# Kernel tuning notes

Hardware: AMD Instinct MI355X
Metric: run time of the kernel (lower is better)

The kernel has to match this reference:

```python
import jax, jax.numpy as jnp
import numpy as np

N = 100000
E = 1600000
IN_C = 128
OUT_C = 64


def setup_inputs() -> dict:
    key = jax.random.key(0)
    ks = jax.random.split(key, 8)
    x = jax.random.normal(ks[0], (N, IN_C), dtype=jnp.float32)
    edge_index = jax.random.randint(ks[1], (2, E), 0, N, dtype=jnp.int64)
    neg_edge_index = jax.random.randint(ks[2], (2, E), 0, N, dtype=jnp.int64)
    # GCNConv params (glorot-ish init)
    W = jax.random.normal(ks[3], (IN_C, OUT_C), dtype=jnp.float32) / np.sqrt(IN_C)
    b = jnp.zeros((OUT_C,), dtype=jnp.float32)
    # classifier Linear(2*out_channels, 2)
    Wc = jax.random.normal(ks[4], (2 * OUT_C, 2), dtype=jnp.float32) / np.sqrt(2 * OUT_C)
    bc = jnp.zeros((2,), dtype=jnp.float32)
    return {"x": x, "edge_index": edge_index, "neg_edge_index": neg_edge_index,
            "W": W, "b": b, "Wc": Wc, "bc": bc}


def gcn_conv(x, edge_index, W, b):
    # Add self-loops, symmetric normalization: D^{-1/2} (A+I) D^{-1/2} X W + b
    loops = jnp.arange(N, dtype=edge_index.dtype)
    src = jnp.concatenate([edge_index[0], loops])  # [E+N]
    dst = jnp.concatenate([edge_index[1], loops])  # [E+N]
    deg = jax.ops.segment_sum(jnp.ones_like(dst, dtype=x.dtype), dst, num_segments=N)
    dinv = jax.lax.rsqrt(jnp.maximum(deg, 1e-12))
    norm = dinv[src] * dinv[dst]                   # [E+N]
    xw = x @ W                                     # [N, OUT_C] transform first (cheaper)
    msg = norm[:, None] * xw[src]                  # gather + scale
    out = jax.ops.segment_sum(msg, dst, num_segments=N)  # scatter-add aggregate
    return out + b


def reference(x, edge_index, neg_edge_index, W, b, Wc, bc):
    h = jax.nn.relu(gcn_conv(x, edge_index, W, b))           # [N, OUT_C]
    total = jnp.concatenate([edge_index, neg_edge_index], axis=1)  # [2, 2E]
    edge_feat = jnp.concatenate([h[total[0]], h[total[1]]], axis=1)  # [2E, 2*OUT_C]
    return edge_feat @ Wc + bc                               # [2E, 2]
```

## Files before the change

### kernel.cpp

```cpp
#include <hip/hip_runtime.h>
#include <stdint.h>

#define N_NODES 100000
#define N_EDGES 1600000
#define IN_C    128
#define OUT_C   64

#define NPB   64
#define NBKT  ((N_NODES + NPB - 1) / NPB)
#define BCAP  1216
#define ACHUNK 8192
#define NABLK ((N_EDGES + ACHUNK - 1) / ACHUNK)

__global__ void zero_kernel(int* __restrict__ cursor) {
    int i = blockIdx.x * blockDim.x + threadIdx.x;
    if (i < NBKT) cursor[i] = 0;
}

__global__ __launch_bounds__(256) void bucketA_kernel(const int* __restrict__ ei,
                                                      int* __restrict__ cursor,
                                                      int* __restrict__ bucket) {
    __shared__ int hist[NBKT];
    __shared__ int base[NBKT];
    __shared__ int hist2[NBKT];
    const int t = threadIdx.x;
    const long long e0 = (long long)blockIdx.x * ACHUNK;
    for (int i = t; i < NBKT; i += 256) { hist[i] = 0; hist2[i] = 0; }
    __syncthreads();
    const int* dsts = ei + N_EDGES;
#pragma unroll
    for (int k = 0; k < ACHUNK / 1024; ++k) {
        long long i4 = e0 / 4 + t + k * 256;
        if (i4 * 4 + 3 < N_EDGES) {
            int4 d = *(const int4*)&dsts[i4 * 4];
            atomicAdd(&hist[d.x >> 6], 1);
            atomicAdd(&hist[d.y >> 6], 1);
            atomicAdd(&hist[d.z >> 6], 1);
            atomicAdd(&hist[d.w >> 6], 1);
        }
    }
    __syncthreads();
    for (int bk = t; bk < NBKT; bk += 256) {
        int c = hist[bk];
        base[bk] = c ? atomicAdd(&cursor[bk], c) : 0;
    }
    __syncthreads();
#pragma unroll
    for (int k = 0; k < ACHUNK / 1024; ++k) {
        long long i4 = e0 / 4 + t + k * 256;
        if (i4 * 4 + 3 < N_EDGES) {
            int4 s4 = *(const int4*)&ei[i4 * 4];
            int4 d4 = *(const int4*)&dsts[i4 * 4];
            int sv[4] = {s4.x, s4.y, s4.z, s4.w};
            int dv[4] = {d4.x, d4.y, d4.z, d4.w};
#pragma unroll
            for (int j = 0; j < 4; ++j) {
                int bk = dv[j] >> 6;
                int pos = base[bk] + atomicAdd(&hist2[bk], 1);
                if (pos < BCAP)
                    bucket[bk * BCAP + pos] = sv[j] * 128 + (dv[j] & (NPB - 1));
            }
        }
    }
}

__global__ __launch_bounds__(256) void bdegcsr_kernel(const int* __restrict__ cursor,
                                                      int* __restrict__ bucket,
                                                      float* __restrict__ dinv,
                                                      int* __restrict__ rowbeg,
                                                      int* __restrict__ rowend) {
    __shared__ int hist[NPB];
    __shared__ int pref[NPB + 1];
    __shared__ int cur[NPB];
    __shared__ int sorted[BCAP];
    const int t = threadIdx.x, b = blockIdx.x;
    if (t < NPB) { hist[t] = 0; cur[t] = 0; }
    __syncthreads();
    int m = cursor[b]; if (m > BCAP) m = BCAP;
    int* bb = bucket + b * BCAP;
    for (int i = t; i < m; i += 256) atomicAdd(&hist[bb[i] & 127], 1);
    __syncthreads();
    if (t == 0) {
        int s = 0;
#pragma unroll
        for (int k = 0; k < NPB; ++k) { pref[k] = s; s += hist[k]; }
        pref[NPB] = s;
    }
    __syncthreads();
    for (int i = t; i < m; i += 256) {
        int e = bb[i];
        int dl = e & 127;
        int pos = pref[dl] + atomicAdd(&cur[dl], 1);
        sorted[pos] = e >> 7;
    }
    __syncthreads();
    for (int i = t; i < m; i += 256) bb[i] = sorted[i];
    if (t < NPB) {
        int n = b * NPB + t;
        if (n < N_NODES) {
            rowbeg[n] = b * BCAP + pref[t];
            rowend[n] = b * BCAP + pref[t + 1];
            dinv[n]   = rsqrtf((float)hist[t] + 1.0f);
        }
    }
}

#define XN  32
#define SXS 132
__global__ __launch_bounds__(256) void xws_kernel(const float* __restrict__ x,
                                                  const float* __restrict__ W,
                                                  const float* __restrict__ dinv,
                                                  float* __restrict__ xws) {
    __shared__ float sW[IN_C * OUT_C];
    __shared__ float sx[XN * SXS];
    const int t = threadIdx.x;
    const int n0 = blockIdx.x * XN;
    const float4* W4 = (const float4*)W;
    float4* sW4 = (float4*)sW;
#pragma unroll
    for (int k = 0; k < 8; ++k) sW4[t + k * 256] = W4[t + k * 256];
#pragma unroll
    for (int k = 0; k < 4; ++k) {
        int idx = (t + k * 256) * 4;
        int r = idx >> 7, kk = idx & 127;
        int n = n0 + r;
        float4 v = (n < N_NODES) ? *(const float4*)&x[(long long)n * IN_C + kk]
                                 : make_float4(0.f, 0.f, 0.f, 0.f);
        *(float4*)&sx[r * SXS + kk] = v;
    }
    __syncthreads();
    const int r  = t >> 4;
    const int cq = (t & 15) << 2;
    float4 a0 = make_float4(0.f,0.f,0.f,0.f), a1 = a0;
#pragma unroll 8
    for (int k = 0; k < IN_C; ++k) {
        float x0 = sx[r * SXS + k];
        float x1 = sx[(r + 16) * SXS + k];
        float4 wv = *(const float4*)&sW[(k << 6) + cq];
        a0.x = fmaf(x0, wv.x, a0.x); a0.y = fmaf(x0, wv.y, a0.y);
        a0.z = fmaf(x0, wv.z, a0.z); a0.w = fmaf(x0, wv.w, a0.w);
        a1.x = fmaf(x1, wv.x, a1.x); a1.y = fmaf(x1, wv.y, a1.y);
        a1.z = fmaf(x1, wv.z, a1.z); a1.w = fmaf(x1, wv.w, a1.w);
    }
    int na = n0 + r, nb = n0 + r + 16;
    if (na < N_NODES) {
        float di = dinv[na];
        a0.x *= di; a0.y *= di; a0.z *= di; a0.w *= di;
        *(float4*)&xws[(long long)na * OUT_C + cq] = a0;
    }
    if (nb < N_NODES) {
        float di = dinv[nb];
        a1.x *= di; a1.y *= di; a1.z *= di; a1.w *= di;
        *(float4*)&xws[(long long)nb * OUT_C + cq] = a1;
    }
}

__global__ __launch_bounds__(256) void aggnode_kernel(
    const int* __restrict__ rowbeg, const int* __restrict__ rowend,
    const int* __restrict__ srcs, const float* __restrict__ dinv,
    const float* __restrict__ xws, const float* __restrict__ b,
    const float* __restrict__ Wc, const float* __restrict__ bc,
    float4* __restrict__ pq) {
    const int lane = threadIdx.x & 63;
    const int node = blockIdx.x * 4 + (threadIdx.x >> 6);
    if (node >= N_NODES) return;
    const int beg = rowbeg[node], end = rowend[node];
    const int c = lane;
    float a0 = 0.f, a1 = 0.f, a2 = 0.f, a3 = 0.f;
    float a4 = 0.f, a5 = 0.f, a6 = 0.f, a7 = 0.f;
    for (int i = beg; i < end; i += 64) {
        int cnt = end - i;
        if (cnt > 64) cnt = 64;
        int sv = (lane < cnt) ? srcs[i + lane] : 0;
        int j = 0;
        for (; j + 7 < cnt; j += 8) {
            int s0 = __shfl(sv, j),     s1 = __shfl(sv, j + 1);
            int s2 = __shfl(sv, j + 2), s3 = __shfl(sv, j + 3);
            int s4 = __shfl(sv, j + 4), s5 = __shfl(sv, j + 5);
            int s6 = __shfl(sv, j + 6), s7 = __shfl(sv, j + 7);
            float x0 = xws[s0 * OUT_C + c], x1 = xws[s1 * OUT_C + c];
            float x2 = xws[s2 * OUT_C + c], x3 = xws[s3 * OUT_C + c];
            float x4 = xws[s4 * OUT_C + c], x5 = xws[s5 * OUT_C + c];
            float x6 = xws[s6 * OUT_C + c], x7 = xws[s7 * OUT_C + c];
            a0 += x0; a1 += x1; a2 += x2; a3 += x3;
            a4 += x4; a5 += x5; a6 += x6; a7 += x7;
        }
        for (; j < cnt; ++j) {
            int s = __shfl(sv, j);
            a0 += xws[s * OUT_C + c];
        }
    }
    float acc = ((a0 + a1) + (a2 + a3)) + ((a4 + a5) + (a6 + a7));
    acc += xws[(long long)node * OUT_C + c];
    float h = fmaxf(fmaf(dinv[node], acc, b[c]), 0.f);
    float p0 = h * Wc[2 * c + 0],           p1 = h * Wc[2 * c + 1];
    float q0 = h * Wc[2 * (OUT_C + c) + 0], q1 = h * Wc[2 * (OUT_C + c) + 1];
#pragma unroll
    for (int off = 32; off; off >>= 1) {
        p0 += __shfl_down(p0, off); p1 += __shfl_down(p1, off);
        q0 += __shfl_down(q0, off); q1 += __shfl_down(q1, off);
    }
    if (lane == 0) pq[node] = make_float4(p0 + bc[0], p1 + bc[1], q0, q1);
}

__global__ void edge_kernel(const int* __restrict__ ei, const int* __restrict__ nei,
                            const float4* __restrict__ pq, float4* __restrict__ out4) {
    int idx = blockIdx.x * blockDim.x + threadIdx.x;
    if (idx >= N_EDGES) return;
    int e2 = idx * 2;
    int2 ss, dd;
    if (e2 < N_EDGES) {
        ss = *(const int2*)&ei[e2];
        dd = *(const int2*)&ei[N_EDGES + e2];
    } else {
        int f = e2 - N_EDGES;
        ss = *(const int2*)&nei[f];
        dd = *(const int2*)&nei[N_EDGES + f];
    }
    float4 pa = pq[ss.x], qa = pq[dd.x];
    float4 pb = pq[ss.y], qb = pq[dd.y];
    out4[idx] = make_float4(pa.x + qa.z, pa.y + qa.w, pb.x + qb.z, pb.y + qb.w);
}

extern "C" void kernel_launch(void* const* d_in, const int* in_sizes, int n_in,
                              void* d_out, int out_size, void* d_ws, size_t ws_size,
                              hipStream_t stream) {
    const float* x   = (const float*)d_in[0];
    const int*   ei  = (const int*)  d_in[1];
    const int*   nei = (const int*)  d_in[2];
    const float* W   = (const float*)d_in[3];
    const float* b   = (const float*)d_in[4];
    const float* Wc  = (const float*)d_in[5];
    const float* bc  = (const float*)d_in[6];

    int*   wsI    = (int*)d_ws;
    float* dinv   = (float*)wsI;
    float* xws    = (float*)(wsI + 100352);
    float* pq     = (float*)(wsI + 6500352);
    int*   cursor = wsI + 6900352;
    int*   rowbeg = wsI + 6901952;
    int*   rowend = wsI + 7002304;
    int*   bucket = wsI + 7102656;

    const int B = 256;
    zero_kernel<<<(NBKT + B - 1) / B, B, 0, stream>>>(cursor);
    bucketA_kernel<<<NABLK, B, 0, stream>>>(ei, cursor, bucket);
    bdegcsr_kernel<<<NBKT, B, 0, stream>>>(cursor, bucket, dinv, rowbeg, rowend);
    xws_kernel<<<(N_NODES + XN - 1) / XN, B, 0, stream>>>(x, W, dinv, xws);
    aggnode_kernel<<<(N_NODES + 3) / 4, B, 0, stream>>>(rowbeg, rowend, bucket, dinv,
                                                        xws, b, Wc, bc, (float4*)pq);
    edge_kernel<<<(N_EDGES + B - 1) / B, B, 0, stream>>>(ei, nei, (const float4*)pq,
                                                         (float4*)d_out);
}
```

Measured before the change: 274.2 us.

## Store transformed features as bf16 and coarsen destination buckets to 1024 nodes

The scaled node features XW·dinv are now stored as packed bf16 pairs, which halves the bytes gathered per edge in the aggregation kernel. Each wavefront half now handles a different neighbor, and each lane accumulates two channels. The bucket sort is coarsened from 64-node buckets to 1024-node super-buckets, and the second pass uses a block-wide scan. This cuts global cursor atomics and bucket count but puts a large sorted array in LDS, which limits occupancy. bf16 rounding of the features adds numeric error.

```diff
diff --git a/kernel.cpp b/kernel.cpp
--- a/kernel.cpp
+++ b/kernel.cpp
@@ -1,31 +1,39 @@
 #include <hip/hip_runtime.h>
-#include <stdint.h>
 
 #define N_NODES 100000
 #define N_EDGES 1600000
 #define IN_C    128
 #define OUT_C   64
 
-#define NPB   64
-#define NBKT  ((N_NODES + NPB - 1) / NPB)
-#define BCAP  1216
+#define SB_NODES 1024
+#define NSB  ((N_NODES + SB_NODES - 1) / SB_NODES)
+#define SCAP 17408
 #define ACHUNK 8192
 #define NABLK ((N_EDGES + ACHUNK - 1) / ACHUNK)
 
+__device__ inline unsigned pack_bf16x2(float lo, float hi) {
+    unsigned a = __float_as_uint(lo), b2 = __float_as_uint(hi);
+    a  += 0x7fff + ((a  >> 16) & 1);
+    b2 += 0x7fff + ((b2 >> 16) & 1);
+    return (a >> 16) | (b2 & 0xffff0000u);
+}
+__device__ inline float bf_lo(unsigned v) { return __uint_as_float(v << 16); }
+__device__ inline float bf_hi(unsigned v) { return __uint_as_float(v & 0xffff0000u); }
+
 __global__ void zero_kernel(int* __restrict__ cursor) {
     int i = blockIdx.x * blockDim.x + threadIdx.x;
-    if (i < NBKT) cursor[i] = 0;
-}
-
-__global__ __launch_bounds__(256) void bucketA_kernel(const int* __restrict__ ei,
-                                                      int* __restrict__ cursor,
-                                                      int* __restrict__ bucket) {
-    __shared__ int hist[NBKT];
-    __shared__ int base[NBKT];
-    __shared__ int hist2[NBKT];
+    if (i < NSB) cursor[i] = 0;
+}
+
+__global__ __launch_bounds__(256) void sorta_kernel(const int* __restrict__ ei,
+                                                    int* __restrict__ cursor,
+                                                    int* __restrict__ sb) {
+    __shared__ int hist[NSB];
+    __shared__ int base_[NSB];
+    __shared__ int cur[NSB];
     const int t = threadIdx.x;
     const long long e0 = (long long)blockIdx.x * ACHUNK;
-    for (int i = t; i < NBKT; i += 256) { hist[i] = 0; hist2[i] = 0; }
+    if (t < NSB) { hist[t] = 0; cur[t] = 0; }
     __syncthreads();
     const int* dsts = ei + N_EDGES;
 #pragma unroll
@@ -33,16 +41,16 @@
         long long i4 = e0 / 4 + t + k * 256;
         if (i4 * 4 + 3 < N_EDGES) {
             int4 d = *(const int4*)&dsts[i4 * 4];
-            atomicAdd(&hist[d.x >> 6], 1);
-            atomicAdd(&hist[d.y >> 6], 1);
-            atomicAdd(&hist[d.z >> 6], 1);
-            atomicAdd(&hist[d.w >> 6], 1);
-        }
-    }
-    __syncthreads();
-    for (int bk = t; bk < NBKT; bk += 256) {
-        int c = hist[bk];
-        base[bk] = c ? atomicAdd(&cursor[bk], c) : 0;
+            atomicAdd(&hist[d.x >> 10], 1);
+            atomicAdd(&hist[d.y >> 10], 1);
+            atomicAdd(&hist[d.z >> 10], 1);
+            atomicAdd(&hist[d.w >> 10], 1);
+        }
+    }
+    __syncthreads();
+    if (t < NSB) {
+        int c = hist[t];
+        base_[t] = c ? atomicAdd(&cursor[t], c) : 0;
     }
     __syncthreads();
 #pragma unroll
@@ -55,52 +63,63 @@
             int dv[4] = {d4.x, d4.y, d4.z, d4.w};
 #pragma unroll
             for (int j = 0; j < 4; ++j) {
-                int bk = dv[j] >> 6;
-                int pos = base[bk] + atomicAdd(&hist2[bk], 1);
-                if (pos < BCAP)
-                    bucket[bk * BCAP + pos] = sv[j] * 128 + (dv[j] & (NPB - 1));
+                int bk = dv[j] >> 10;
+                int pos = base_[bk] + atomicAdd(&cur[bk], 1);
+                if (pos < SCAP)
+                    sb[bk * SCAP + pos] = sv[j] * SB_NODES + (dv[j] & (SB_NODES - 1));
             }
         }
     }
 }
 
-__global__ __launch_bounds__(256) void bdegcsr_kernel(const int* __restrict__ cursor,
-                                                      int* __restrict__ bucket,
-                                                      float* __restrict__ dinv,
-                                                      int* __restrict__ rowbeg,
-                                                      int* __restrict__ rowend) {
-    __shared__ int hist[NPB];
-    __shared__ int pref[NPB + 1];
-    __shared__ int cur[NPB];
-    __shared__ int sorted[BCAP];
+__global__ __launch_bounds__(256) void sortb_kernel(const int* __restrict__ cursor,
+                                                    int* __restrict__ sb,
+                                                    float* __restrict__ dinv,
+                                                    int* __restrict__ rowbeg,
+                                                    int* __restrict__ rowend) {
+    __shared__ int hist[SB_NODES];
+    __shared__ int pref[SB_NODES + 1];
+    __shared__ int cur[SB_NODES];
+    __shared__ int sc[256];
+    __shared__ int sorted[SCAP];
     const int t = threadIdx.x, b = blockIdx.x;
-    if (t < NPB) { hist[t] = 0; cur[t] = 0; }
-    __syncthreads();
-    int m = cursor[b]; if (m > BCAP) m = BCAP;
-    int* bb = bucket + b * BCAP;
-    for (int i = t; i < m; i += 256) atomicAdd(&hist[bb[i] & 127], 1);
-    __syncthreads();
-    if (t == 0) {
-        int s = 0;
-#pragma unroll
-        for (int k = 0; k < NPB; ++k) { pref[k] = s; s += hist[k]; }
-        pref[NPB] = s;
-    }
+    for (int k = t; k < SB_NODES; k += 256) { hist[k] = 0; cur[k] = 0; }
+    __syncthreads();
+    int m = cursor[b]; if (m > SCAP) m = SCAP;
+    int* bb = sb + b * SCAP;
+    for (int i = t; i < m; i += 256) atomicAdd(&hist[bb[i] & (SB_NODES - 1)], 1);
+    __syncthreads();
+    int c0 = hist[4 * t], c1 = hist[4 * t + 1], c2 = hist[4 * t + 2], c3 = hist[4 * t + 3];
+    int tsum = c0 + c1 + c2 + c3;
+    sc[t] = tsum;
+    __syncthreads();
+    for (int off = 1; off < 256; off <<= 1) {
+        int u = (t >= off) ? sc[t - off] : 0;
+        __syncthreads();
+        sc[t] += u;
+        __syncthreads();
+    }
+    int excl = sc[t] - tsum;
+    pref[4 * t]     = excl;
+    pref[4 * t + 1] = excl + c0;
+    pref[4 * t + 2] = excl + c0 + c1;
+    pref[4 * t + 3] = excl + c0 + c1 + c2;
+    if (t == 255) pref[SB_NODES] = sc[255];
     __syncthreads();
     for (int i = t; i < m; i += 256) {
         int e = bb[i];
-        int dl = e & 127;
+        int dl = e & (SB_NODES - 1);
         int pos = pref[dl] + atomicAdd(&cur[dl], 1);
-        sorted[pos] = e >> 7;
+        sorted[pos] = e >> 10;
     }
     __syncthreads();
     for (int i = t; i < m; i += 256) bb[i] = sorted[i];
-    if (t < NPB) {
-        int n = b * NPB + t;
+    for (int k = t; k < SB_NODES; k += 256) {
+        int n = b * SB_NODES + k;
         if (n < N_NODES) {
-            rowbeg[n] = b * BCAP + pref[t];
-            rowend[n] = b * BCAP + pref[t + 1];
-            dinv[n]   = rsqrtf((float)hist[t] + 1.0f);
+            rowbeg[n] = b * SCAP + pref[k];
+            rowend[n] = b * SCAP + pref[k + 1];
+            dinv[n]   = rsqrtf((float)hist[k] + 1.0f);
         }
     }
 }
@@ -110,7 +129,7 @@
 __global__ __launch_bounds__(256) void xws_kernel(const float* __restrict__ x,
                                                   const float* __restrict__ W,
                                                   const float* __restrict__ dinv,
-                                                  float* __restrict__ xws) {
+                                                  unsigned* __restrict__ xwsh) {
     __shared__ float sW[IN_C * OUT_C];
     __shared__ float sx[XN * SXS];
     const int t = threadIdx.x;
@@ -145,58 +164,79 @@
     int na = n0 + r, nb = n0 + r + 16;
     if (na < N_NODES) {
         float di = dinv[na];
-        a0.x *= di; a0.y *= di; a0.z *= di; a0.w *= di;
-        *(float4*)&xws[(long long)na * OUT_C + cq] = a0;
+        uint2 o = make_uint2(pack_bf16x2(a0.x * di, a0.y * di),
+                             pack_bf16x2(a0.z * di, a0.w * di));
+        *(uint2*)&xwsh[(long long)na * 32 + ((t & 15) << 1)] = o;
     }
     if (nb < N_NODES) {
         float di = dinv[nb];
-        a1.x *= di; a1.y *= di; a1.z *= di; a1.w *= di;
-        *(float4*)&xws[(long long)nb * OUT_C + cq] = a1;
+        uint2 o = make_uint2(pack_bf16x2(a1.x * di, a1.y * di),
+                             pack_bf16x2(a1.z * di, a1.w * di));
+        *(uint2*)&xwsh[(long long)nb * 32 + ((t & 15) << 1)] = o;
     }
 }
 
 __global__ __launch_bounds__(256) void aggnode_kernel(
     const int* __restrict__ rowbeg, const int* __restrict__ rowend,
     const int* __restrict__ srcs, const float* __restrict__ dinv,
-    const float* __restrict__ xws, const float* __restrict__ b,
+    const unsigned* __restrict__ xwsh, const float* __restrict__ b,
     const float* __restrict__ Wc, const float* __restrict__ bc,
     float4* __restrict__ pq) {
     const int lane = threadIdx.x & 63;
     const int node = blockIdx.x * 4 + (threadIdx.x >> 6);
     if (node >= N_NODES) return;
     const int beg = rowbeg[node], end = rowend[node];
-    const int c = lane;
-    float a0 = 0.f, a1 = 0.f, a2 = 0.f, a3 = 0.f;
-    float a4 = 0.f, a5 = 0.f, a6 = 0.f, a7 = 0.f;
+    const int half = lane >> 5, hl = lane & 31;
+    float ax0 = 0.f, ay0 = 0.f, ax1 = 0.f, ay1 = 0.f;
+    float ax2 = 0.f, ay2 = 0.f, ax3 = 0.f, ay3 = 0.f;
     for (int i = beg; i < end; i += 64) {
         int cnt = end - i;
         if (cnt > 64) cnt = 64;
         int sv = (lane < cnt) ? srcs[i + lane] : 0;
         int j = 0;
-        for (; j + 7 < cnt; j += 8) {
-            int s0 = __shfl(sv, j),     s1 = __shfl(sv, j + 1);
-            int s2 = __shfl(sv, j + 2), s3 = __shfl(sv, j + 3);
-            int s4 = __shfl(sv, j + 4), s5 = __shfl(sv, j + 5);
-            int s6 = __shfl(sv, j + 6), s7 = __shfl(sv, j + 7);
-            float x0 = xws[s0 * OUT_C + c], x1 = xws[s1 * OUT_C + c];
-            float x2 = xws[s2 * OUT_C + c], x3 = xws[s3 * OUT_C + c];
-            float x4 = xws[s4 * OUT_C + c], x5 = xws[s5 * OUT_C + c];
-            float x6 = xws[s6 * OUT_C + c], x7 = xws[s7 * OUT_C + c];
-            a0 += x0; a1 += x1; a2 += x2; a3 += x3;
-            a4 += x4; a5 += x5; a6 += x6; a7 += x7;
-        }
-        for (; j < cnt; ++j) {
+        for (; j + 15 < cnt; j += 16) {
+#pragma unroll
+            for (int u = 0; u < 8; ++u) {
+                int s = __shfl(sv, j + 2 * u + half);
+                unsigned v = xwsh[s * 32 + hl];
+                float lo = bf_lo(v), hi = bf_hi(v);
+                if (u == 0 || u == 4) { ax0 += lo; ay0 += hi; }
+                else if (u == 1 || u == 5) { ax1 += lo; ay1 += hi; }
+                else if (u == 2 || u == 6) { ax2 += lo; ay2 += hi; }
+                else { ax3 += lo; ay3 += hi; }
+            }
+        }
+        for (; j + 1 < cnt; j += 2) {
+            int s = __shfl(sv, j + half);
+            unsigned v = xwsh[s * 32 + hl];
+            ax0 += bf_lo(v); ay0 += bf_hi(v);
+        }
+        if (j < cnt) {
             int s = __shfl(sv, j);
-            a0 += xws[s * OUT_C + c];
-        }
-    }
-    float acc = ((a0 + a1) + (a2 + a3)) + ((a4 + a5) + (a6 + a7));
-    acc += xws[(long long)node * OUT_C + c];
-    float h = fmaxf(fmaf(dinv[node], acc, b[c]), 0.f);
-    float p0 = h * Wc[2 * c + 0],           p1 = h * Wc[2 * c + 1];
-    float q0 = h * Wc[2 * (OUT_C + c) + 0], q1 = h * Wc[2 * (OUT_C + c) + 1];
-#pragma unroll
-    for (int off = 32; off; off >>= 1) {
+            if (lane < 32) {
+                unsigned v = xwsh[s * 32 + hl];
+                ax1 += bf_lo(v); ay1 += bf_hi(v);
+            }
+        }
+    }
+    float ax = (ax0 + ax1) + (ax2 + ax3);
+    float ay = (ay0 + ay1) + (ay2 + ay3);
+    ax += __shfl(ax, lane + 32);
+    ay += __shfl(ay, lane + 32);
+    unsigned vs = xwsh[node * 32 + hl];
+    ax += bf_lo(vs); ay += bf_hi(vs);
+    float di = dinv[node];
+    float2 b2 = ((const float2*)b)[hl];
+    float h0 = fmaxf(fmaf(di, ax, b2.x), 0.f);
+    float h1 = fmaxf(fmaf(di, ay, b2.y), 0.f);
+    float4 wcs = ((const float4*)Wc)[hl];
+    float4 wcd = ((const float4*)(Wc + 2 * OUT_C))[hl];
+    float p0 = h0 * wcs.x + h1 * wcs.z;
+    float p1 = h0 * wcs.y + h1 * wcs.w;
+    float q0 = h0 * wcd.x + h1 * wcd.z;
+    float q1 = h0 * wcd.y + h1 * wcd.w;
+#pragma unroll
+    for (int off = 16; off; off >>= 1) {
         p0 += __shfl_down(p0, off); p1 += __shfl_down(p1, off);
         q0 += __shfl_down(q0, off); q1 += __shfl_down(q1, off);
     }
@@ -233,22 +273,22 @@
     const float* Wc  = (const float*)d_in[5];
     const float* bc  = (const float*)d_in[6];
 
-    int*   wsI    = (int*)d_ws;
-    float* dinv   = (float*)wsI;
-    float* xws    = (float*)(wsI + 100352);
-    float* pq     = (float*)(wsI + 6500352);
-    int*   cursor = wsI + 6900352;
-    int*   rowbeg = wsI + 6901952;
-    int*   rowend = wsI + 7002304;
-    int*   bucket = wsI + 7102656;
+    int*      wsI    = (int*)d_ws;
+    float*    dinv   = (float*)wsI;
+    unsigned* xwsh   = (unsigned*)(wsI + 100352);
+    float*    pq     = (float*)(wsI + 3300352);
+    int*      cursor = wsI + 3700352;
+    int*      rowbeg = wsI + 3700480;
+    int*      rowend = wsI + 3800832;
+    int*      sbuf   = wsI + 3901184;
 
     const int B = 256;
-    zero_kernel<<<(NBKT + B - 1) / B, B, 0, stream>>>(cursor);
-    bucketA_kernel<<<NABLK, B, 0, stream>>>(ei, cursor, bucket);
-    bdegcsr_kernel<<<NBKT, B, 0, stream>>>(cursor, bucket, dinv, rowbeg, rowend);
-    xws_kernel<<<(N_NODES + XN - 1) / XN, B, 0, stream>>>(x, W, dinv, xws);
-    aggnode_kernel<<<(N_NODES + 3) / 4, B, 0, stream>>>(rowbeg, rowend, bucket, dinv,
-                                                        xws, b, Wc, bc, (float4*)pq);
+    zero_kernel<<<1, B, 0, stream>>>(cursor);
+    sorta_kernel<<<NABLK, B, 0, stream>>>(ei, cursor, sbuf);
+    sortb_kernel<<<NSB, B, 0, stream>>>(cursor, sbuf, dinv, rowbeg, rowend);
+    xws_kernel<<<(N_NODES + XN - 1) / XN, B, 0, stream>>>(x, W, dinv, xwsh);
+    aggnode_kernel<<<(N_NODES + 3) / 4, B, 0, stream>>>(rowbeg, rowend, sbuf, dinv,
+                                                        xwsh, b, Wc, bc, (float4*)pq);
     edge_kernel<<<(N_EDGES + B - 1) / B, B, 0, stream>>>(ei, nei, (const float4*)pq,
                                                          (float4*)d_out);
 }
```

Result: no change. 270.6 us (-1.3%).
